# Kernel tuning notes

Measured on AMD Instinct MI355X. Metric: run time of the kernel, lower is better.

The kernel has to match this reference:

```python
import jax, jax.numpy as jnp
import numpy as np

# pywt db4 decomposition filters (w.dec_lo / w.dec_hi), full precision
DEC_LO = np.array([-0.010597401784997278, 0.032883011666982945, 0.030841381835986965,
                   -0.18703481171888114, -0.02798376941698385, 0.6308807679295904,
                   0.7148465705525415, 0.23037781330885523], dtype=np.float32)
DEC_HI = np.array([-0.23037781330885523, 0.7148465705525415, -0.6308807679295904,
                   -0.02798376941698385, 0.18703481171888114, 0.030841381835986965,
                   -0.032883011666982945, -0.010597401784997278], dtype=np.float32)
FLEN = 8
LEVELS = 4
# kernel for lax correlation == pywt convolution => use reversed dec filters
_KERN = np.stack([DEC_LO[::-1], DEC_HI[::-1]])[:, None, :]  # [2, 1, F]


def _dwt_step(x):
    """Single-level DWT matching pywt.dwt(x, 'db4', mode='symmetric').
    x: [N, L] -> (cA, cD) each [N, (L+F-1)//2].
    pywt: symmetric-extend by F-1 per side, full convolution with dec filter,
    keep conv[F-1:-(F-1)][1::2]  ==  correlation(ext[:,1:], reversed_filter, stride 2).
    """
    ext = jnp.pad(x, ((0, 0), (FLEN - 1, FLEN - 1)), mode='symmetric')[:, 1:]
    out = jax.lax.conv_general_dilated(
        ext[:, None, :],                      # [N, 1, Lext-1]
        jnp.asarray(_KERN, dtype=x.dtype),    # [2, 1, F]
        window_strides=(2,), padding='VALID') # [N, 2, o]
    return out[:, 0, :], out[:, 1, :]


def _features(c):
    """6 statistical features per signal. c: [N, L] -> [N, 6]."""
    absc = jnp.abs(c)
    sq = c * c
    mean_abs = absc.mean(-1)
    std = jnp.std(c, axis=-1)               # population std, matches np.std
    rms = jnp.sqrt(sq.mean(-1))
    mx = absc.max(-1)
    energy = sq.sum(-1)
    zc = (jnp.diff(jnp.sign(c), axis=-1) != 0).sum(-1).astype(c.dtype) / c.shape[-1]
    return jnp.stack([mean_abs, std, rms, mx, energy, zc], axis=-1)


def _wavelet_features(x2d):
    """x2d: [N, T] -> [N, 6*(LEVELS+1)] in pywt.wavedec coeff order."""
    cA = x2d
    cds = []
    for _ in range(LEVELS):
        cA, cD = _dwt_step(cA)
        cds.append(cD)
    coeffs = [cA] + cds[::-1]  # [cA4, cD4, cD3, cD2, cD1]
    return jnp.concatenate([_features(c) for c in coeffs], axis=-1)


def setup_inputs() -> dict:
    key = jax.random.key(0)
    x = jax.random.normal(key, (64, 64, 16384), dtype=jnp.float32)
    return {"x": x}


def reference(x):
    B, C, T = x.shape
    feats = _wavelet_features(x.reshape(B * C, T))  # [B*C, 30]
    return feats.reshape(B, C, -1)                  # [B, C, 30]
```

## Files before the change

### kernel.cpp

```cpp
#include <hip/hip_runtime.h>


#define T0 16384
#define BLK 512
#define NW (BLK / 64)

constexpr float FLO[8] = {
     0.23037781330885523f,  0.7148465705525415f,   0.6308807679295904f,
    -0.02798376941698385f, -0.18703481171888114f,  0.030841381835986965f,
     0.032883011666982945f, -0.010597401784997278f };
constexpr float FHI[8] = {
    -0.010597401784997278f, -0.032883011666982945f, 0.030841381835986965f,
     0.18703481171888114f,  -0.02798376941698385f,  -0.6308807679295904f,
     0.7148465705525415f,   -0.23037781330885523f };

__device__ __forceinline__ float getsym(const float* __restrict__ s, int t, int L) {
    if (t < 0) t = -1 - t;
    else if (t >= L) t = 2 * L - 1 - t;
    return s[t];
}

__device__ __forceinline__ float zcstep(float p, float q) {
    return ((__float_as_int(p) ^ __float_as_int(q)) < 0) ? 1.f : 0.f;
}

__device__ __forceinline__ void band_reduce(float sabs, float ssum, float ssq,
                                            float smax, float zc,
                                            int band, float* __restrict__ red) {
    #pragma unroll
    for (int off = 32; off > 0; off >>= 1) {
        sabs += __shfl_xor(sabs, off, 64);
        ssum += __shfl_xor(ssum, off, 64);
        ssq  += __shfl_xor(ssq,  off, 64);
        smax  = fmaxf(smax, __shfl_xor(smax, off, 64));
        zc   += __shfl_xor(zc,   off, 64);
    }
    const int lane = threadIdx.x & 63;
    const int wave = threadIdx.x >> 6;
    if (lane == 0) {
        float* r = red + (band * NW + wave) * 5;
        r[0] = sabs; r[1] = ssum; r[2] = ssq; r[3] = smax; r[4] = zc;
    }
}

template<bool LAST>
__device__ __forceinline__ void dwt_quad_level(const float* __restrict__ src, int L,
                                               float* __restrict__ dst, int o,
                                               int dband, float* __restrict__ red) {
    float sabs = 0.f, ssum = 0.f, ssq = 0.f, smax = 0.f, zc = 0.f;
    float sabsA = 0.f, ssumA = 0.f, ssqA = 0.f, smaxA = 0.f, zcA = 0.f;
    const int nq_main = (o - 1) >> 2;

    for (int k = threadIdx.x; k < nq_main; k += BLK) {
        const int w = 8 * k - 8;
        float v[20];
        if (w >= 0 && w + 20 <= L) {
            #pragma unroll
            for (int q = 0; q < 5; ++q) {
                const float4 t = *reinterpret_cast<const float4*>(src + w + 4 * q);
                v[4*q+0] = t.x; v[4*q+1] = t.y; v[4*q+2] = t.z; v[4*q+3] = t.w;
            }
        } else {
            #pragma unroll
            for (int j = 2; j < 18; ++j) v[j] = getsym(src, w + j, L);
        }
        float a[5], d[5];
        #pragma unroll
        for (int i = 0; i < 5; ++i) { a[i] = 0.f; d[i] = 0.f; }
        #pragma unroll
        for (int i = 0; i < 4; ++i) {
            #pragma unroll
            for (int m = 0; m < 8; ++m) {
                a[i] = fmaf(v[2*i+2+m], FLO[m], a[i]);
                d[i] = fmaf(v[2*i+2+m], FHI[m], d[i]);
            }
        }
        #pragma unroll
        for (int m = 0; m < 8; ++m) {
            d[4] = fmaf(v[10+m], FHI[m], d[4]);
            if constexpr (LAST) a[4] = fmaf(v[10+m], FLO[m], a[4]);
        }
        if constexpr (!LAST) {
            *reinterpret_cast<float4*>(dst + 4 * k) = make_float4(a[0], a[1], a[2], a[3]);
        }
        #pragma unroll
        for (int i = 0; i < 4; ++i) {
            const float ad = fabsf(d[i]);
            sabs += ad; ssum += d[i]; ssq = fmaf(d[i], d[i], ssq);
            smax = fmaxf(smax, ad);
            zc += zcstep(d[i], d[i+1]);
            if constexpr (LAST) {
                const float aa = fabsf(a[i]);
                sabsA += aa; ssumA += a[i]; ssqA = fmaf(a[i], a[i], ssqA);
                smaxA = fmaxf(smaxA, aa);
                zcA += zcstep(a[i], a[i+1]);
            }
        }
    }

    if (threadIdx.x == BLK - 1) {
        const int k = nq_main;
        const int w = 8 * k - 8;
        float v[20];
        #pragma unroll
        for (int j = 2; j < 18; ++j) v[j] = getsym(src, w + j, L);
        float a[5], d[5];
        #pragma unroll
        for (int i = 0; i < 5; ++i) { a[i] = 0.f; d[i] = 0.f; }
        #pragma unroll
        for (int i = 0; i < 5; ++i) {
            #pragma unroll
            for (int m = 0; m < 8; ++m) {
                a[i] = fmaf(v[2*i+2+m], FLO[m], a[i]);
                d[i] = fmaf(v[2*i+2+m], FHI[m], d[i]);
            }
        }
        #pragma unroll
        for (int i = 0; i < 4; ++i) {
            const int p = 4 * k + i;
            if (p < o) {
                const float ad = fabsf(d[i]);
                sabs += ad; ssum += d[i]; ssq = fmaf(d[i], d[i], ssq);
                smax = fmaxf(smax, ad);
                if (p + 1 < o) zc += zcstep(d[i], d[i+1]);
                if constexpr (LAST) {
                    const float aa = fabsf(a[i]);
                    sabsA += aa; ssumA += a[i]; ssqA = fmaf(a[i], a[i], ssqA);
                    smaxA = fmaxf(smaxA, aa);
                    if (p + 1 < o) zcA += zcstep(a[i], a[i+1]);
                } else {
                    dst[p] = a[i];
                }
            }
        }
    }

    band_reduce(sabs, ssum, ssq, smax, zc, dband, red);
    if constexpr (LAST) band_reduce(sabsA, ssumA, ssqA, smaxA, zcA, 0, red);
}

__global__ void __launch_bounds__(BLK, 6)
wavelet_feat_kernel(const float* __restrict__ x, float* __restrict__ out) {
    __shared__ __align__(16) float A[8196];
    __shared__ __align__(16) float B[4104];
    __shared__ float red[5 * NW * 5];

    const int sig = blockIdx.x;
    const float* src0 = x + (size_t)sig * T0;
    float* outp = out + (size_t)sig * 30;

    dwt_quad_level<false>(src0, T0,   A, 8195, 4, red);
    __syncthreads();
    dwt_quad_level<false>(A,    8195, B, 4101, 3, red);
    __syncthreads();
    dwt_quad_level<false>(B,    4101, A, 2054, 2, red);
    __syncthreads();
    dwt_quad_level<true >(A,    2054, nullptr, 1030, 1, red);
    __syncthreads();

    if (threadIdx.x < 5) {
        const int band = threadIdx.x;
        float a = 0.f, s = 0.f, q = 0.f, m = 0.f, z = 0.f;
        #pragma unroll
        for (int w = 0; w < NW; ++w) {
            const float* r = red + (band * NW + w) * 5;
            a += r[0]; s += r[1]; q += r[2]; m = fmaxf(m, r[3]); z += r[4];
        }
        const int o = (band <= 1) ? 1030 : (band == 2 ? 2054 : (band == 3 ? 4101 : 8195));
        const float inv  = 1.0f / (float)o;
        const float mean = s * inv;
        const float var  = q * inv - mean * mean;
        float* op = outp + band * 6;
        op[0] = a * inv;
        op[1] = sqrtf(fmaxf(var, 0.f));
        op[2] = sqrtf(q * inv);
        op[3] = m;
        op[4] = q;
        op[5] = z * inv;
    }
}

extern "C" void kernel_launch(void* const* d_in, const int* in_sizes, int n_in,
                              void* d_out, int out_size, void* d_ws, size_t ws_size,
                              hipStream_t stream) {
    const float* x = (const float*)d_in[0];
    float* out = (float*)d_out;
    const int nsig = in_sizes[0] / T0;
    hipLaunchKernelGGL(wavelet_feat_kernel, dim3(nsig), dim3(BLK), 0, stream, x, out);
}
```

Before: 90.06 us.

## Share next-output via lane shuffle, template level sizes, bitmask zero-crossings, parallel final reduce

Each thread now gets the fifth detail/approx coefficient it needs for the zero-crossing count from its neighbour lane by shuffle, instead of computing a redundant fifth 8-tap output. It recomputes that value only on lane 63 or at the loop end. Level lengths become template constants so the main loop can be unrolled when the trip count divides the block size. Zero crossings are counted with a sign bitmask and popcount. The wave reduction stops at four lanes per wave and the cross-wave finish is done by five waves with shuffles, which adds shuffle traffic and shared-memory slots.

```diff
diff --git a/kernel.cpp b/kernel.cpp
--- a/kernel.cpp
+++ b/kernel.cpp
@@ -28,83 +28,115 @@
                                             float smax, float zc,
                                             int band, float* __restrict__ red) {
     #pragma unroll
-    for (int off = 32; off > 0; off >>= 1) {
+    for (int off = 32; off >= 4; off >>= 1) {
         sabs += __shfl_xor(sabs, off, 64);
         ssum += __shfl_xor(ssum, off, 64);
         ssq  += __shfl_xor(ssq,  off, 64);
         smax  = fmaxf(smax, __shfl_xor(smax, off, 64));
         zc   += __shfl_xor(zc,   off, 64);
     }
-    const int lane = threadIdx.x & 63;
-    const int wave = threadIdx.x >> 6;
-    if (lane == 0) {
-        float* r = red + (band * NW + wave) * 5;
+    const int lane = (int)threadIdx.x & 63;
+    if (lane < 4) {
+        const int wave = (int)threadIdx.x >> 6;
+        float* r = red + ((band * NW + wave) * 4 + lane) * 5;
         r[0] = sabs; r[1] = ssum; r[2] = ssq; r[3] = smax; r[4] = zc;
     }
 }
 
-template<bool LAST>
-__device__ __forceinline__ void dwt_quad_level(const float* __restrict__ src, int L,
-                                               float* __restrict__ dst, int o,
-                                               int dband, float* __restrict__ red) {
+__device__ __forceinline__ void load_win(const float* __restrict__ src, int L, int k,
+                                         float* __restrict__ v) {
+    const int w = 8 * k - 8;
+    if (w >= 0 && w + 20 <= L) {
+        #pragma unroll
+        for (int q = 0; q < 5; ++q) {
+            const float4 t = *reinterpret_cast<const float4*>(src + w + 4 * q);
+            v[4*q+0] = t.x; v[4*q+1] = t.y; v[4*q+2] = t.z; v[4*q+3] = t.w;
+        }
+    } else {
+        #pragma unroll
+        for (int j = 2; j < 18; ++j) v[j] = getsym(src, w + j, L);
+    }
+}
+
+template<bool LAST, int L, int o, int DBAND>
+__device__ __forceinline__ void dwt_level(const float* __restrict__ src,
+                                          float* __restrict__ dst,
+                                          float* __restrict__ red) {
+    constexpr int NQ = (o - 1) >> 2;
+    const int tid = (int)threadIdx.x;
+    const bool l63 = (tid & 63) == 63;
     float sabs = 0.f, ssum = 0.f, ssq = 0.f, smax = 0.f, zc = 0.f;
     float sabsA = 0.f, ssumA = 0.f, ssqA = 0.f, smaxA = 0.f, zcA = 0.f;
-    const int nq_main = (o - 1) >> 2;
-
-    for (int k = threadIdx.x; k < nq_main; k += BLK) {
-        const int w = 8 * k - 8;
+
+    auto body = [&](int k) {
         float v[20];
-        if (w >= 0 && w + 20 <= L) {
+        load_win(src, L, k, v);
+        float a0=0.f,a1=0.f,a2=0.f,a3=0.f,d0=0.f,d1=0.f,d2=0.f,d3=0.f;
+        #pragma unroll
+        for (int m = 0; m < 8; ++m) {
+            const float lo = FLO[m], hi = FHI[m];
+            a0 = fmaf(v[2+m], lo, a0);  d0 = fmaf(v[2+m], hi, d0);
+            a1 = fmaf(v[4+m], lo, a1);  d1 = fmaf(v[4+m], hi, d1);
+            a2 = fmaf(v[6+m], lo, a2);  d2 = fmaf(v[6+m], hi, d2);
+            a3 = fmaf(v[8+m], lo, a3);  d3 = fmaf(v[8+m], hi, d3);
+        }
+        float dn = __shfl_down(d0, 1, 64);
+        float an = 0.f;
+        if constexpr (LAST) an = __shfl_down(a0, 1, 64);
+        if (l63 || k + 1 >= NQ) {
+            float t = 0.f;
             #pragma unroll
-            for (int q = 0; q < 5; ++q) {
-                const float4 t = *reinterpret_cast<const float4*>(src + w + 4 * q);
-                v[4*q+0] = t.x; v[4*q+1] = t.y; v[4*q+2] = t.z; v[4*q+3] = t.w;
+            for (int m = 0; m < 8; ++m) t = fmaf(v[10+m], FHI[m], t);
+            dn = t;
+            if constexpr (LAST) {
+                float u = 0.f;
+                #pragma unroll
+                for (int m = 0; m < 8; ++m) u = fmaf(v[10+m], FLO[m], u);
+                an = u;
             }
-        } else {
-            #pragma unroll
-            for (int j = 2; j < 18; ++j) v[j] = getsym(src, w + j, L);
-        }
-        float a[5], d[5];
-        #pragma unroll
-        for (int i = 0; i < 5; ++i) { a[i] = 0.f; d[i] = 0.f; }
-        #pragma unroll
-        for (int i = 0; i < 4; ++i) {
-            #pragma unroll
-            for (int m = 0; m < 8; ++m) {
-                a[i] = fmaf(v[2*i+2+m], FLO[m], a[i]);
-                d[i] = fmaf(v[2*i+2+m], FHI[m], d[i]);
-            }
-        }
-        #pragma unroll
-        for (int m = 0; m < 8; ++m) {
-            d[4] = fmaf(v[10+m], FHI[m], d[4]);
-            if constexpr (LAST) a[4] = fmaf(v[10+m], FLO[m], a[4]);
-        }
-        if constexpr (!LAST) {
-            *reinterpret_cast<float4*>(dst + 4 * k) = make_float4(a[0], a[1], a[2], a[3]);
-        }
-        #pragma unroll
-        for (int i = 0; i < 4; ++i) {
-            const float ad = fabsf(d[i]);
-            sabs += ad; ssum += d[i]; ssq = fmaf(d[i], d[i], ssq);
-            smax = fmaxf(smax, ad);
-            zc += zcstep(d[i], d[i+1]);
-            if constexpr (LAST) {
-                const float aa = fabsf(a[i]);
-                sabsA += aa; ssumA += a[i]; ssqA = fmaf(a[i], a[i], ssqA);
-                smaxA = fmaxf(smaxA, aa);
-                zcA += zcstep(a[i], a[i+1]);
-            }
-        }
-    }
-
-    if (threadIdx.x == BLK - 1) {
-        const int k = nq_main;
-        const int w = 8 * k - 8;
-        float v[20];
-        #pragma unroll
-        for (int j = 2; j < 18; ++j) v[j] = getsym(src, w + j, L);
-        float a[5], d[5];
+        }
+        if constexpr (!LAST)
+            *reinterpret_cast<float4*>(dst + 4 * k) = make_float4(a0, a1, a2, a3);
+        sabs += fabsf(d0) + fabsf(d1) + fabsf(d2) + fabsf(d3);
+        ssum += d0 + d1 + d2 + d3;
+        ssq = fmaf(d0, d0, ssq); ssq = fmaf(d1, d1, ssq);
+        ssq = fmaf(d2, d2, ssq); ssq = fmaf(d3, d3, ssq);
+        smax = fmaxf(smax, fmaxf(fmaxf(fabsf(d0), fabsf(d1)),
+                                 fmaxf(fabsf(d2), fabsf(d3))));
+        unsigned mk = (__float_as_uint(d0) >> 31)
+                    | ((__float_as_uint(d1) >> 31) << 1)
+                    | ((__float_as_uint(d2) >> 31) << 2)
+                    | ((__float_as_uint(d3) >> 31) << 3)
+                    | ((__float_as_uint(dn) >> 31) << 4);
+        zc += (float)__popc((mk ^ (mk >> 1)) & 15u);
+        if constexpr (LAST) {
+            sabsA += fabsf(a0) + fabsf(a1) + fabsf(a2) + fabsf(a3);
+            ssumA += a0 + a1 + a2 + a3;
+            ssqA = fmaf(a0, a0, ssqA); ssqA = fmaf(a1, a1, ssqA);
+            ssqA = fmaf(a2, a2, ssqA); ssqA = fmaf(a3, a3, ssqA);
+            smaxA = fmaxf(smaxA, fmaxf(fmaxf(fabsf(a0), fabsf(a1)),
+                                       fmaxf(fabsf(a2), fabsf(a3))));
+            unsigned ma = (__float_as_uint(a0) >> 31)
+                        | ((__float_as_uint(a1) >> 31) << 1)
+                        | ((__float_as_uint(a2) >> 31) << 2)
+                        | ((__float_as_uint(a3) >> 31) << 3)
+                        | ((__float_as_uint(an) >> 31) << 4);
+            zcA += (float)__popc((ma ^ (ma >> 1)) & 15u);
+        }
+    };
+
+    if constexpr ((NQ % BLK) == 0) {
+        #pragma unroll 2
+        for (int c = 0; c < NQ / BLK; ++c) body(c * BLK + tid);
+    } else {
+        for (int k = tid; k < NQ; k += BLK) body(k);
+    }
+
+    if (tid == BLK - 1) {
+        constexpr int k = NQ;
+        float v[20], a[5], d[5];
+        #pragma unroll
+        for (int j = 2; j < 18; ++j) v[j] = getsym(src, 8 * k - 8 + j, L);
         #pragma unroll
         for (int i = 0; i < 5; ++i) { a[i] = 0.f; d[i] = 0.f; }
         #pragma unroll
@@ -119,14 +151,12 @@
         for (int i = 0; i < 4; ++i) {
             const int p = 4 * k + i;
             if (p < o) {
-                const float ad = fabsf(d[i]);
-                sabs += ad; ssum += d[i]; ssq = fmaf(d[i], d[i], ssq);
-                smax = fmaxf(smax, ad);
+                sabs += fabsf(d[i]); ssum += d[i]; ssq = fmaf(d[i], d[i], ssq);
+                smax = fmaxf(smax, fabsf(d[i]));
                 if (p + 1 < o) zc += zcstep(d[i], d[i+1]);
                 if constexpr (LAST) {
-                    const float aa = fabsf(a[i]);
-                    sabsA += aa; ssumA += a[i]; ssqA = fmaf(a[i], a[i], ssqA);
-                    smaxA = fmaxf(smaxA, aa);
+                    sabsA += fabsf(a[i]); ssumA += a[i]; ssqA = fmaf(a[i], a[i], ssqA);
+                    smaxA = fmaxf(smaxA, fabsf(a[i]));
                     if (p + 1 < o) zcA += zcstep(a[i], a[i+1]);
                 } else {
                     dst[p] = a[i];
@@ -135,7 +165,7 @@
         }
     }
 
-    band_reduce(sabs, ssum, ssq, smax, zc, dband, red);
+    band_reduce(sabs, ssum, ssq, smax, zc, DBAND, red);
     if constexpr (LAST) band_reduce(sabsA, ssumA, ssqA, smaxA, zcA, 0, red);
 }
 
@@ -143,40 +173,49 @@
 wavelet_feat_kernel(const float* __restrict__ x, float* __restrict__ out) {
     __shared__ __align__(16) float A[8196];
     __shared__ __align__(16) float B[4104];
-    __shared__ float red[5 * NW * 5];
-
-    const int sig = blockIdx.x;
-    const float* src0 = x + (size_t)sig * T0;
-    float* outp = out + (size_t)sig * 30;
-
-    dwt_quad_level<false>(src0, T0,   A, 8195, 4, red);
-    __syncthreads();
-    dwt_quad_level<false>(A,    8195, B, 4101, 3, red);
-    __syncthreads();
-    dwt_quad_level<false>(B,    4101, A, 2054, 2, red);
-    __syncthreads();
-    dwt_quad_level<true >(A,    2054, nullptr, 1030, 1, red);
-    __syncthreads();
-
-    if (threadIdx.x < 5) {
-        const int band = threadIdx.x;
+    __shared__ float red[5 * 32 * 5];
+
+    const float* src0 = x + (size_t)blockIdx.x * T0;
+    float* outp = out + (size_t)blockIdx.x * 30;
+
+    dwt_level<false, 16384, 8195, 4>(src0, A, red);
+    __syncthreads();
+    dwt_level<false,  8195, 4101, 3>(A,    B, red);
+    __syncthreads();
+    dwt_level<false,  4101, 2054, 2>(B,    A, red);
+    __syncthreads();
+    dwt_level<true,   2054, 1030, 1>(A, nullptr, red);
+    __syncthreads();
+
+    const int wave = (int)threadIdx.x >> 6, lane = (int)threadIdx.x & 63;
+    if (wave < 5) {
         float a = 0.f, s = 0.f, q = 0.f, m = 0.f, z = 0.f;
-        #pragma unroll
-        for (int w = 0; w < NW; ++w) {
-            const float* r = red + (band * NW + w) * 5;
-            a += r[0]; s += r[1]; q += r[2]; m = fmaxf(m, r[3]); z += r[4];
-        }
-        const int o = (band <= 1) ? 1030 : (band == 2 ? 2054 : (band == 3 ? 4101 : 8195));
-        const float inv  = 1.0f / (float)o;
-        const float mean = s * inv;
-        const float var  = q * inv - mean * mean;
-        float* op = outp + band * 6;
-        op[0] = a * inv;
-        op[1] = sqrtf(fmaxf(var, 0.f));
-        op[2] = sqrtf(q * inv);
-        op[3] = m;
-        op[4] = q;
-        op[5] = z * inv;
+        if (lane < 32) {
+            const float* r = red + (wave * 32 + lane) * 5;
+            a = r[0]; s = r[1]; q = r[2]; m = r[3]; z = r[4];
+        }
+        #pragma unroll
+        for (int off = 16; off > 0; off >>= 1) {
+            a += __shfl_xor(a, off, 64);
+            s += __shfl_xor(s, off, 64);
+            q += __shfl_xor(q, off, 64);
+            m  = fmaxf(m, __shfl_xor(m, off, 64));
+            z += __shfl_xor(z, off, 64);
+        }
+        if (lane == 0) {
+            const int band = wave;
+            const int o = (band <= 1) ? 1030 : (band == 2 ? 2054 : (band == 3 ? 4101 : 8195));
+            const float inv  = 1.0f / (float)o;
+            const float mean = s * inv;
+            const float var  = q * inv - mean * mean;
+            float* op = outp + band * 6;
+            op[0] = a * inv;
+            op[1] = sqrtf(fmaxf(var, 0.f));
+            op[2] = sqrtf(q * inv);
+            op[3] = m;
+            op[4] = q;
+            op[5] = z * inv;
+        }
     }
 }
 
```

After: 127.9 us. 1.42x slower.
